# Performance work log

Hardware: AMD Instinct MI355X
Metric: run time of the kernel (lower is better)

Reference implementation:

```python
import jax, jax.numpy as jnp
import numpy as np

B, N, D = 8, 500, 256
H, W = 480, 640
NUM_CORNERS = 500
MATCH_RADIUS = 1.0
SCORE_RADIUS = 8
BETA = (1.0, 1.0, 1.0)


def _rodrigues(aa):
    theta = jnp.linalg.norm(aa, axis=-1, keepdims=True)
    k = aa / jnp.maximum(theta, 1e-8)
    kx, ky, kz = k[..., 0], k[..., 1], k[..., 2]
    z = jnp.zeros_like(kx)
    Km = jnp.stack([jnp.stack([z, -kz, ky], -1),
                    jnp.stack([kz, z, -kx], -1),
                    jnp.stack([-ky, kx, z], -1)], -2)
    th = theta[..., None]
    return jnp.eye(3) + jnp.sin(th) * Km + (1. - jnp.cos(th)) * (Km @ Km)


def setup_inputs() -> dict:
    key = jax.random.key(0)
    ks = jax.random.split(key, 8)
    descriptors = jax.random.normal(ks[0], (B, N, D), jnp.float32)
    points = jax.random.uniform(ks[1], (B, N, 2), jnp.float32, -1.0, 1.0)
    pointness = jax.random.uniform(ks[2], (B, 1, H, W), jnp.float32) * 0.98 + 0.01
    depths_dense = jax.random.uniform(ks[3], (B, 1, H, W), jnp.float32) * 4.0 + 1.0
    imgs = jax.random.uniform(ks[4], (B, 3, H, W), jnp.float32)
    aa = jax.random.normal(ks[5], (B, 3), jnp.float32) * 0.02
    t = jax.random.normal(ks[6], (B, 3), jnp.float32) * 0.05
    R = _rodrigues(aa)
    poses = jnp.tile(jnp.eye(4, dtype=jnp.float32), (B, 1, 1))
    poses = poses.at[:, :3, :3].set(R).at[:, :3, 3].set(t)
    Kmat = jnp.tile(jnp.array([[300., 0., W / 2.], [0., 300., H / 2.], [0., 0., 1.]], jnp.float32), (B, 1, 1))
    return {"descriptors": descriptors, "points": points, "pointness": pointness,
            "depths_dense": depths_dense, "poses": poses, "K": Kmat, "imgs": imgs}


def denormalize(pts, h, w):
    return jnp.stack([(pts[..., 0] + 1.) * 0.5 * (w - 1), (pts[..., 1] + 1.) * 0.5 * (h - 1)], -1)


def normalize_pix(pts, h, w):
    return jnp.stack([2. * pts[..., 0] / (w - 1) - 1., 2. * pts[..., 1] / (h - 1) - 1.], -1)


def bilinear_sample(img, px):  # img (H,W), px (...,2) pixel coords
    x = jnp.clip(px[..., 0], 0., W - 1.)
    y = jnp.clip(px[..., 1], 0., H - 1.)
    x0 = jnp.floor(x); y0 = jnp.floor(y)
    x1 = jnp.minimum(x0 + 1., W - 1.); y1 = jnp.minimum(y0 + 1., H - 1.)
    wx = x - x0; wy = y - y0
    x0i = x0.astype(jnp.int32); x1i = x1.astype(jnp.int32)
    y0i = y0.astype(jnp.int32); y1i = y1.astype(jnp.int32)
    v00 = img[y0i, x0i]; v01 = img[y0i, x1i]
    v10 = img[y1i, x0i]; v11 = img[y1i, x1i]
    return v00 * (1 - wx) * (1 - wy) + v01 * wx * (1 - wy) + v10 * (1 - wx) * wy + v11 * wx * wy


def pairwise_project(pts, depths, poses, Kmat):
    # pts (B,N,2) normalized; proj[i,j] = points of frame i projected into frame j
    px = denormalize(pts, H, W)
    d = jax.vmap(bilinear_sample)(depths[:, 0], px)  # (B,Np)
    Kinv = jnp.linalg.inv(Kmat)
    homog = jnp.concatenate([px, jnp.ones_like(px[..., :1])], -1)
    Xc = d[..., None] * jnp.einsum('bij,bnj->bni', Kinv, homog)
    Rm = poses[:, :3, :3]; t = poses[:, :3, 3]
    Xw = jnp.einsum('bij,bnj->bni', Rm, Xc) + t[:, None, :]
    diff = Xw[:, None, :, :] - t[None, :, None, :]           # (src,dst,Np,3)
    Xj = jnp.einsum('jba,ijnb->ijna', Rm, diff)              # R_j^T (Xw - t_j)
    uvw = jnp.einsum('jab,ijnb->ijna', Kmat, Xj)
    z = uvw[..., 2]
    zs = jnp.where(jnp.abs(z) < 1e-6, 1e-6, z)
    pn = normalize_pix(jnp.stack([uvw[..., 0] / zs, uvw[..., 1] / zs], -1), H, W)
    invis = (z <= 1e-6) | (jnp.abs(pn[..., 0]) > 1.) | (jnp.abs(pn[..., 1]) > 1.) | (d[:, None, :] <= 0.)
    return pn, invis


def conv2d_same(x, k):
    return jax.lax.conv_general_dilated(x, k[None, None].astype(x.dtype), (1, 1), 'SAME')


_SOBEL_X = np.array([[-1, 0, 1], [-2, 0, 2], [-1, 0, 1]], np.float32) / 8.


def _gauss_kernel(size=7, sigma=1.0):
    r = np.arange(size) - size // 2
    g = np.exp(-r ** 2 / (2 * sigma ** 2)); g /= g.sum()
    return np.outer(g, g).astype(np.float32)


_GAUSS = _gauss_kernel()


def gftt_response(gray):  # min-eigenvalue (Shi-Tomasi) corner response
    gx = conv2d_same(gray, jnp.asarray(_SOBEL_X))
    gy = conv2d_same(gray, jnp.asarray(_SOBEL_X.T))
    g = jnp.asarray(_GAUSS)
    dx2 = conv2d_same(gx * gx, g)
    dy2 = conv2d_same(gy * gy, g)
    dxy = conv2d_same(gx * gy, g)
    tr = dx2 + dy2
    det = dx2 * dy2 - dxy * dxy
    return 0.5 * (tr - jnp.sqrt(jnp.clip(tr * tr - 4. * det, 0.)))


def nms2d(x, k=5):
    mp = jax.lax.reduce_window(x, -jnp.inf, jax.lax.max, (1, 1, k, k), (1, 1, 1, 1), 'SAME')
    return x * (x == mp).astype(x.dtype)


def get_corners(imgs, depths, poses, Kmat):
    gray = (0.299 * imgs[:, 0] + 0.587 * imgs[:, 1] + 0.114 * imgs[:, 2])[:, None]
    c = nms2d(gftt_response(gray))
    r = SCORE_RADIUS
    blocks = c.reshape(B, 1, H // r, r, W // r, r)  # unfold/fold with stride==kernel
    bm = blocks.max(axis=(3, 5), keepdims=True)
    blocks = blocks * ((blocks > 0) & (blocks == bm)).astype(c.dtype)
    c = blocks.reshape(B, 1, H, W)
    vals, idx = jax.lax.top_k(c.reshape(B, -1), NUM_CORNERS)
    xs = (idx % W).astype(jnp.float32)
    ys = (idx // W).astype(jnp.float32)
    coords = normalize_pix(jnp.stack([xs, ys], -1), H, W)
    proj, invis = pairwise_project(coords, depths, poses, Kmat)
    proj = jnp.where(invis[..., None], -2.0, proj)
    combined = jnp.transpose(proj, (1, 0, 2, 3)).reshape(B, B * NUM_CORNERS, 2)  # per dst frame
    pix = jnp.round(denormalize(combined, H, W)).astype(jnp.int32)
    wq, hq = pix[..., 0], pix[..., 1]
    valid = wq >= 0
    v = jnp.tile(vals.reshape(-1), B).reshape(B, B * NUM_CORNERS)
    v = jnp.where(valid, v, 0.)
    hc = jnp.clip(hq, 0, H - 1)
    wc = jnp.clip(wq, 0, W - 1)
    bidx = jnp.broadcast_to(jnp.arange(B)[:, None], (B, B * NUM_CORNERS))
    target = jnp.zeros((B, H, W), imgs.dtype).at[bidx, hc, wc].max(v)
    target = nms2d(target[:, None])
    return (target > 0).astype(imgs.dtype)


def distinction_loss(desc):
    dn = desc / jnp.clip(jnp.linalg.norm(desc, axis=-1, keepdims=True), 1e-8)
    c = jnp.einsum('bnd,bmd->bnm', dn, dn)
    return jax.nn.relu(c).mean()


def match_loss(desc, points, proj, invis):
    p_src = denormalize(jax.lax.stop_gradient(points), H, W)  # (B,N,2)
    p_dst = denormalize(jax.lax.stop_gradient(proj), H, W)    # (src a, dst b, N, 2)
    diff = p_src[None, :, :, None, :] - p_dst[:, :, None, :, :]  # (a,b,n,m,2)
    m = (diff ** 2).sum(-1) <= MATCH_RADIUS ** 2
    m = m & (~invis)[:, :, :, None]                 # zero invisible rows
    n_idx = jnp.arange(N)
    m = m & (n_idx[:, None] < n_idx[None, :])       # triu(diagonal=1)
    dn = desc / jnp.clip(jnp.linalg.norm(desc, axis=-1, keepdims=True), 1e-8)
    cos = jnp.einsum('bnd,amd->abnm', dn, dn)       # cosine(desc[b,n], desc[a,m])
    mf = m.astype(desc.dtype)
    cnt = jnp.maximum(mf.sum(), 1.)
    return ((1. - cos) * mf).sum() / cnt


def bce(p, t):
    logp = jnp.maximum(jnp.log(p), -100.)
    log1p = jnp.maximum(jnp.log(1. - p), -100.)
    return -(t * logp + (1. - t) * log1p).mean()


def reference(descriptors, points, pointness, depths_dense, poses, K, imgs):
    distinction = distinction_loss(descriptors)
    target = get_corners(imgs, depths_dense, poses, K)
    cornerness = bce(pointness, target)
    proj, invis = pairwise_project(points, depths_dense, poses, K)
    match = match_loss(descriptors, points, proj, invis)
    return BETA[0] * distinction + BETA[1] * cornerness + BETA[2] * match
```

## Files before the change

kernel.cpp:

```cpp
#include <hip/hip_runtime.h>
#include <math.h>

#define BB 8
#define NN 500
#define DDIM 256
#define HH 480
#define WW 640
#define HWSZ (HH*WW)
#define BHW (BB*HWSZ)
#define NBLK 4800
#define NOVF 3392
#define NLIST (BB*NN*BB)
#define NBCE2 512
#define NCORR 125
#define NDM 66

#define PD_DIST  0
#define PD_MS    512
#define PD_MC    1024
#define PD_BCE   1536
#define PD_CORR  2560
#define PD_TOTAL 2688

typedef __attribute__((ext_vector_type(8))) short short8;
typedef __attribute__((ext_vector_type(4))) float f32x4;


static __device__ __forceinline__ float wredmaxf(float v) {
  #pragma unroll
  for (int o = 1; o < 64; o <<= 1) v = fmaxf(v, __shfl_xor(v, o, 64));
  return v;
}

static __device__ __forceinline__ double blockRedSum256(double v) {
  __shared__ double sp[4];
  __syncthreads();
  #pragma unroll
  for (int o = 32; o > 0; o >>= 1) v += __shfl_down(v, o, 64);
  int lane = threadIdx.x & 63, wid = threadIdx.x >> 6;
  if (lane == 0) sp[wid] = v;
  __syncthreads();
  double r = 0.0;
  if (threadIdx.x == 0) r = sp[0] + sp[1] + sp[2] + sp[3];
  return r;
}

static __device__ __forceinline__ unsigned short f2bf(float f) {
  unsigned u = __float_as_uint(f);
  return (unsigned short)((u + 0x7FFFu + ((u >> 16) & 1u)) >> 16);
}

static __device__ __forceinline__ float bilin(const float* __restrict__ img, float px, float py) {
  float x = fminf(fmaxf(px, 0.0f), 639.0f);
  float y = fminf(fmaxf(py, 0.0f), 479.0f);
  float x0 = floorf(x), y0 = floorf(y);
  float x1 = fminf(x0 + 1.0f, 639.0f);
  float y1 = fminf(y0 + 1.0f, 479.0f);
  float wx = x - x0, wy = y - y0;
  int x0i = (int)x0, x1i = (int)x1, y0i = (int)y0, y1i = (int)y1;
  float v00 = img[y0i*WW + x0i], v01 = img[y0i*WW + x1i];
  float v10 = img[y1i*WW + x0i], v11 = img[y1i*WW + x1i];
  return v00*(1.0f-wx)*(1.0f-wy) + v01*wx*(1.0f-wy) + v10*(1.0f-wx)*wy + v11*wx*wy;
}

static __device__ void src_compute(float px, float py, const float* __restrict__ dep,
                                   const float* __restrict__ poses, const float* __restrict__ Km,
                                   int bimg, float* Xw, float* dout) {
  float d = bilin(dep, px, py);
  const float* Kb = Km + bimg*9;
  double a00=Kb[0],a01=Kb[1],a02=Kb[2],a10=Kb[3],a11=Kb[4],a12=Kb[5],a20=Kb[6],a21=Kb[7],a22=Kb[8];
  double det = a00*(a11*a22-a12*a21) - a01*(a10*a22-a12*a20) + a02*(a10*a21-a11*a20);
  double id = 1.0/det;
  float i00=(float)((a11*a22-a12*a21)*id), i01=(float)((a02*a21-a01*a22)*id), i02=(float)((a01*a12-a02*a11)*id);
  float i10=(float)((a12*a20-a10*a22)*id), i11=(float)((a00*a22-a02*a20)*id), i12=(float)((a02*a10-a00*a12)*id);
  float i20=(float)((a10*a21-a11*a20)*id), i21=(float)((a01*a20-a00*a21)*id), i22=(float)((a00*a11-a01*a10)*id);
  float c0 = i00*px + i01*py + i02;
  float c1 = i10*px + i11*py + i12;
  float c2 = i20*px + i21*py + i22;
  float X0 = d*c0, X1 = d*c1, X2 = d*c2;
  const float* P = poses + bimg*16;
  Xw[0] = (P[0]*X0 + P[1]*X1 + P[2]*X2)  + P[3];
  Xw[1] = (P[4]*X0 + P[5]*X1 + P[6]*X2)  + P[7];
  Xw[2] = (P[8]*X0 + P[9]*X1 + P[10]*X2) + P[11];
  *dout = d;
}

static __device__ void project_to(const float* __restrict__ poses, const float* __restrict__ Km,
                                  int j, const float* Xw, float dsrc,
                                  float* pnx, float* pny, bool* invis) {
  const float* P = poses + j*16;
  float d0 = Xw[0]-P[3], d1 = Xw[1]-P[7], d2 = Xw[2]-P[11];
  float Xj0 = P[0]*d0 + P[4]*d1 + P[8]*d2;
  float Xj1 = P[1]*d0 + P[5]*d1 + P[9]*d2;
  float Xj2 = P[2]*d0 + P[6]*d1 + P[10]*d2;
  const float* Kb = Km + j*9;
  float u = Kb[0]*Xj0 + Kb[1]*Xj1 + Kb[2]*Xj2;
  float v = Kb[3]*Xj0 + Kb[4]*Xj1 + Kb[5]*Xj2;
  float z = Kb[6]*Xj0 + Kb[7]*Xj1 + Kb[8]*Xj2;
  float zs = (fabsf(z) < 1e-6f) ? 1e-6f : z;
  float pu = u/zs, pv = v/zs;
  float nx = 2.0f*pu/639.0f - 1.0f;
  float ny = 2.0f*pv/479.0f - 1.0f;
  *pnx = nx; *pny = ny;
  *invis = (z <= 1e-6f) || (fabsf(nx) > 1.0f) || (fabsf(ny) > 1.0f) || (dsrc <= 0.0f);
}


__global__ __launch_bounds__(256) void k_front(const float* __restrict__ imgs, float* __restrict__ resp,
                                               int* __restrict__ ovf, int* __restrict__ list,
                                               unsigned int* __restrict__ dnb_u, int* __restrict__ done,
                                               const float* __restrict__ desc, float* __restrict__ dn,
                                               unsigned short* __restrict__ dnb,
                                               const float* __restrict__ points, const float* __restrict__ depths,
                                               const float* __restrict__ poses, const float* __restrict__ Km,
                                               float* __restrict__ psrc, float* __restrict__ pdst,
                                               int* __restrict__ minv,
                                               const float* __restrict__ pn, double* __restrict__ pd) {
  __shared__ float smem[6536];
  __shared__ float Gw[7];
  int bid = blockIdx.x, tid = threadIdx.x;
  if (bid < 2400) {
    float* sgxy = smem;
    float* gray = smem + 2888;
    float* hxx  = smem + 2888;
    float* hyy  = hxx + 1216;
    float* hxy  = hyy + 1216;
    int b = bid / 300, r = bid % 300;
    int byi = r / 20, bxi = r % 20;
    int bx = bxi*32, by = byi*32;
    int tx = tid & 31, ty = tid >> 5;
    if (bid < 20) {
      int g = bid*256 + tid;
      if (g == 0) *done = 0;
      for (int e = g; e < BB*64; e += 20*256) ovf[e] = 0;
      for (int e = g; e < NLIST; e += 20*256) list[e] = -1;
      for (int e = g; e < 12288; e += 20*256) {
        int bi = e / 1536, rr2 = e % 1536;
        dnb_u[(bi*512 + 500)*128 + rr2] = 0u;
      }
    }
    if (tid < 7) {
      double g[7]; double s = 0.0;
      for (int q = 0; q < 7; q++) { double rr2 = (double)(q-3); g[q] = exp(-(rr2*rr2)/2.0); s += g[q]; }
      Gw[tid] = (float)(g[tid]/s);
    }
    const float* ib = imgs + (size_t)b*3*HWSZ;
    for (int ly = ty; ly < 40; ly += 8) {
      int Y = by - 4 + ly;
      bool yin = (Y >= 0 && Y < HH);
      for (int lx = tx; lx < 40; lx += 32) {
        int X = bx - 4 + lx;
        float v = 0.f;
        if (yin && X >= 0 && X < WW) {
          int p = Y*WW + X;
          v = 0.299f*ib[p] + 0.587f*ib[HWSZ+p] + 0.114f*ib[2*HWSZ+p];
        }
        gray[ly*41+lx] = v;
      }
    }
    __syncthreads();
    const float kxw[3][3] = {{-0.125f,0.f,0.125f},{-0.25f,0.f,0.25f},{-0.125f,0.f,0.125f}};
    for (int ly = ty; ly < 38; ly += 8) {
      int Y = by - 3 + ly;
      bool yin = (Y >= 0 && Y < HH);
      for (int lx = tx; lx < 38; lx += 32) {
        int X = bx - 3 + lx;
        float sx = 0.f, sy = 0.f;
        #pragma unroll
        for (int i = 0; i < 3; i++)
          #pragma unroll
          for (int j = 0; j < 3; j++) {
            float v = gray[(ly+i)*41 + (lx+j)];
            sx += kxw[i][j]*v;
            sy += kxw[j][i]*v;
          }
        bool in = yin && (X >= 0 && X < WW);
        int e = ly*38 + lx;
        sgxy[e*2]   = in ? sx : 0.f;
        sgxy[e*2+1] = in ? sy : 0.f;
      }
    }
    __syncthreads();
    for (int rr2 = ty; rr2 < 38; rr2 += 8) {
      int base = (rr2*38 + tx)*2;
      float axx = 0.f, ayy = 0.f, axy = 0.f;
      #pragma unroll
      for (int j = 0; j < 7; j++) {
        float a = sgxy[base + j*2];
        float c = sgxy[base + j*2 + 1];
        float Gj = Gw[j];
        axx += Gj*(a*a); ayy += Gj*(c*c); axy += Gj*(a*c);
      }
      int e = rr2*32 + tx;
      hxx[e] = axx; hyy[e] = ayy; hxy[e] = axy;
    }
    __syncthreads();
    int r0 = ty*4;
    float axx[4] = {0,0,0,0}, ayy[4] = {0,0,0,0}, axy[4] = {0,0,0,0};
    #pragma unroll
    for (int rr2 = 0; rr2 < 10; rr2++) {
      int rr3 = r0 + rr2;
      float vxx = hxx[rr3*32+tx], vyy = hyy[rr3*32+tx], vxy = hxy[rr3*32+tx];
      #pragma unroll
      for (int o = 0; o < 4; o++) {
        int i = rr2 - o;
        if (i >= 0 && i <= 6) {
          float Gi = Gw[i];
          axx[o] += Gi*vxx; ayy[o] += Gi*vyy; axy[o] += Gi*vxy;
        }
      }
    }
    #pragma unroll
    for (int o = 0; o < 4; o++) {
      float tr = axx[o] + ayy[o];
      float det = axx[o]*ayy[o] - axy[o]*axy[o];
      float disc = fmaxf(tr*tr - 4.0f*det, 0.f);
      int y = by + r0 + o;
      resp[(size_t)b*HWSZ + y*WW + (bx+tx)] = 0.5f*(tr - sqrtf(disc));
    }
  } else if (bid < 3400) {
    int row = (bid - 2400)*4 + (tid >> 6);
    int lane = tid & 63;
    float4 v4 = *(const float4*)&desc[(size_t)row*DDIM + lane*4];
    float s = v4.x*v4.x + v4.y*v4.y + v4.z*v4.z + v4.w*v4.w;
    #pragma unroll
    for (int o = 32; o > 0; o >>= 1) s += __shfl_down(s, o, 64);
    s = __shfl(s, 0, 64);
    float den = fmaxf(sqrtf(s), 1e-8f);
    float4 o4 = make_float4(v4.x/den, v4.y/den, v4.z/den, v4.w/den);
    *(float4*)&dn[(size_t)row*DDIM + lane*4] = o4;
    int pr = (row/500)*512 + (row%500);
    unsigned lo = (unsigned)f2bf(o4.x) | ((unsigned)f2bf(o4.y) << 16);
    unsigned hi = (unsigned)f2bf(o4.z) | ((unsigned)f2bf(o4.w) << 16);
    *(uint2*)&dnb[(size_t)pr*DDIM + lane*4] = make_uint2(lo, hi);
  } else if (bid < 3416) {
    int t = (bid - 3400)*256 + tid;
    if (t < BB*NN) {
      int a = t / NN, m = t % NN;
      float p0 = points[t*2], p1 = points[t*2+1];
      float px = (p0 + 1.0f)*0.5f*639.0f;
      float py = (p1 + 1.0f)*0.5f*479.0f;
      float Xw[3], d;
      src_compute(px, py, depths + (size_t)a*HWSZ, poses, Km, a, Xw, &d);
      psrc[t*2] = px; psrc[t*2+1] = py;
      for (int b = 0; b < BB; b++) {
        float nx, ny; bool inv;
        project_to(poses, Km, b, Xw, d, &nx, &ny, &inv);
        int o = (a*BB + b)*NN + m;
        pdst[o*2]   = (nx + 1.0f)*0.5f*639.0f;
        pdst[o*2+1] = (ny + 1.0f)*0.5f*479.0f;
        minv[o] = inv ? 1 : 0;
      }
    }
  } else {
    int blk = bid - 3416;
    int g = blk*256 + tid;
    double l = 0.0;
    for (int q = g; q < BHW/4; q += NBCE2*256) {
      float4 v = ((const float4*)pn)[q];
      l -= (double)fmaxf(logf(1.f - v.x), -100.f);
      l -= (double)fmaxf(logf(1.f - v.y), -100.f);
      l -= (double)fmaxf(logf(1.f - v.z), -100.f);
      l -= (double)fmaxf(logf(1.f - v.w), -100.f);
    }
    double s = blockRedSum256(l);
    if (tid == 0) pd[PD_BCE + blk] = s;
  }
}

__global__ __launch_bounds__(256) void k_mid(const float* __restrict__ resp, float* __restrict__ cv,
                                             int* __restrict__ ci, float* __restrict__ cvo,
                                             int* __restrict__ cio, int* __restrict__ ovf,
                                             float* __restrict__ target,
                                             const float* __restrict__ psrc, const float* __restrict__ pdst,
                                             const int* __restrict__ minv, const float* __restrict__ dn,
                                             const short* __restrict__ dnb, double* __restrict__ pd) {
  __shared__ float sbuf[3508];
  int bid = blockIdx.x, tid = threadIdx.x;
  if (bid < NDM) {
    int w = tid >> 6, lane = tid & 63;
    int gw = bid*4 + w;
    int r16 = lane & 15, koff = (lane >> 4)*8;
    double dsum = 0.0;
    for (int j = 0; j < 16; j++) {
      int jb = gw*16 + j;
      int b = jb / 528, t = jb % 528;
      int I = (int)((sqrtf(8.f*(float)t + 1.f) - 1.f)*0.5f);
      while ((I+1)*(I+2)/2 <= t) I++;
      while (I*(I+1)/2 > t) I--;
      int J = t - I*(I+1)/2;
      const short* bp = dnb + (size_t)b*512*DDIM;
      const short* ap = bp + (I*16 + r16)*DDIM + koff;
      const short* cp = bp + (J*16 + r16)*DDIM + koff;
      f32x4 acc = {0.f, 0.f, 0.f, 0.f};
      #pragma unroll
      for (int kk = 0; kk < 8; kk++) {
        short8 af = *(const short8*)(ap + kk*32);
        short8 bf = *(const short8*)(cp + kk*32);
        acc = __builtin_amdgcn_mfma_f32_16x16x32_bf16(af, bf, acc, 0, 0, 0);
      }
      float ls = fmaxf(acc[0],0.f) + fmaxf(acc[1],0.f) + fmaxf(acc[2],0.f) + fmaxf(acc[3],0.f);
      dsum += (double)ls * ((I == J) ? 1.0 : 2.0);
    }
    double s = blockRedSum256(dsum);
    if (tid == 0) pd[PD_DIST + bid] = s;
  } else if (bid < NDM + 512) {
    int mbid = bid - NDM;
    float* spd = sbuf;
    float* ssrc = sbuf + 1000;
    int* sinv = (int*)(sbuf + 2000);
    int ab = mbid & 63; int b = ab % BB; int a = ab / BB;
    int ys = mbid >> 6;
    for (int e = tid; e < NN; e += 256) {
      spd[e*2]   = pdst[(ab*NN+e)*2];
      spd[e*2+1] = pdst[(ab*NN+e)*2+1];
      sinv[e]    = minv[ab*NN+e];
      ssrc[e*2]   = psrc[(b*NN+e)*2];
      ssrc[e*2+1] = psrc[(b*NN+e)*2+1];
    }
    __syncthreads();
    double lsum = 0.0, lcnt = 0.0;
    for (int mm = ys; mm < NN; mm += 8) {
      float px = spd[mm*2], py = spd[mm*2+1];
      for (int nn = tid; nn < mm; nn += 256) {
        if (sinv[nn]) continue;
        float dx = ssrc[nn*2]   - px;
        float dy = ssrc[nn*2+1] - py;
        if (dx*dx + dy*dy <= 1.0f) {
          const float* da = dn + ((size_t)a*NN + mm)*DDIM;
          const float* db = dn + ((size_t)b*NN + nn)*DDIM;
          float dot = 0.f;
          for (int q = 0; q < DDIM; q++) dot += db[q]*da[q];
          lsum += (double)(1.0f - dot);
          lcnt += 1.0;
        }
      }
    }
    double s = blockRedSum256(lsum);
    if (tid == 0) pd[PD_MS + mbid] = s;
    double c2 = blockRedSum256(lcnt);
    if (tid == 0) pd[PD_MC + mbid] = c2;
  } else {
    int nb = bid - (NDM + 512);
    int b = nb / 300, r = nb % 300;
    int byi = r / 20, bxi = r % 20;
    int bx = bxi*32, by = byi*32;
    float* s = sbuf;
    float* hm = sbuf + 1332;
    float* c32 = sbuf + 2484;
    const float* rp = resp + (size_t)b*HWSZ;
    for (int e = tid; e < 36*36; e += 256) {
      int ly = e/36, lx = e%36;
      int X = bx - 2 + lx, Y = by - 2 + ly;
      s[ly*37+lx] = (X>=0 && X<WW && Y>=0 && Y<HH) ? rp[Y*WW+X] : -INFINITY;
    }
    __syncthreads();
    for (int e = tid; e < 36*32; e += 256) {
      int rr = e >> 5, co = e & 31;
      int base = rr*37 + co;
      float m = s[base];
      m = fmaxf(m, s[base+1]); m = fmaxf(m, s[base+2]);
      m = fmaxf(m, s[base+3]); m = fmaxf(m, s[base+4]);
      hm[e] = m;
    }
    __syncthreads();
    for (int e = tid; e < 1024; e += 256) {
      int y = e >> 5, x = e & 31;
      float mp = hm[y*32+x];
      mp = fmaxf(mp, hm[(y+1)*32+x]); mp = fmaxf(mp, hm[(y+2)*32+x]);
      mp = fmaxf(mp, hm[(y+3)*32+x]); mp = fmaxf(mp, hm[(y+4)*32+x]);
      float v = s[(y+2)*37 + (x+2)];
      c32[e] = (v == mp) ? v : 0.f;
      target[(size_t)b*HWSZ + (by+y)*WW + (bx+x)] = 0.f;
    }
    __syncthreads();
    int wv = tid >> 6, lane = tid & 63;
    int ly8 = lane >> 3, lx8 = lane & 7;
    for (int q = 0; q < 4; q++) {
      int bb = wv*4 + q;
      int oy = (bb >> 2)*8, ox = (bb & 3)*8;
      float cval = c32[(oy+ly8)*32 + ox+lx8];
      float bm = wredmaxf(cval);
      bool win = (cval > 0.f) && (cval == bm);
      unsigned long long mask = __ballot(win);
      int BY = byi*4 + (bb >> 2), BX = bxi*4 + (bb & 3);
      int rblk = BY*80 + BX;
      int gidx = (by+oy+ly8)*WW + (bx+ox+lx8);
      if (mask == 0ull) {
        if (lane == 0) { cv[b*NBLK+rblk] = 0.f; ci[b*NBLK+rblk] = 0; }
      } else if (win) {
        int rank = __popcll(mask & ((1ull << lane) - 1ull));
        if (rank == 0) { cv[b*NBLK+rblk] = cval; ci[b*NBLK+rblk] = gidx; }
        else {
          int pos = atomicAdd(&ovf[b*64], 1);
          if (pos < NOVF) { cvo[b*NOVF+pos] = cval; cio[b*NOVF+pos] = gidx; }
        }
      }
    }
  }
}

__global__ __launch_bounds__(1024) void k_topscat(const float* __restrict__ cv, const int* __restrict__ ci,
                                                  const float* __restrict__ cvo, const int* __restrict__ cio,
                                                  const int* __restrict__ ovf,
                                                  const float* __restrict__ depths, const float* __restrict__ poses,
                                                  const float* __restrict__ Km,
                                                  unsigned int* __restrict__ target, int* __restrict__ list) {
  __shared__ unsigned int hist[16*257];
  __shared__ unsigned int histsum[256];
  __shared__ unsigned long long prefix_s;
  __shared__ int kk_s, fin_s, cgt_s, ceq_s;
  __shared__ float s_topv[NN];
  __shared__ int s_topi[NN];
  int b = blockIdx.x;
  int tid = threadIdx.x;
  int w257 = (tid >> 6)*257;
  int nval = min(ovf[b*64], NOVF);
  unsigned long long kreg[8];
  #pragma unroll
  for (int q = 0; q < 8; q++) {
    int e = tid + q*1024;
    float v = 0.f; unsigned int idx = 0u;
    if (e < NBLK) { v = cv[b*NBLK+e]; idx = (unsigned int)ci[b*NBLK+e]; }
    else if (e - NBLK < nval) { v = cvo[b*NOVF+e-NBLK]; idx = (unsigned int)cio[b*NOVF+e-NBLK]; }
    kreg[q] = ((unsigned long long)__float_as_uint(v) << 32) | (0xFFFFFFFFu - idx);
  }
  if (tid == 0) { prefix_s = 0ull; kk_s = NN; fin_s = -1; cgt_s = 0; ceq_s = 0; }
  for (int e = tid; e < 16*257; e += 1024) hist[e] = 0u;
  __syncthreads();
  for (int round = 0; round < 8; round++) {
    int shift = 56 - 8*round;
    unsigned long long prefix = prefix_s;
    int kk = kk_s;
    unsigned long long himask = (round == 0) ? 0ull : (~0ull << (shift + 8));
    #pragma unroll
    for (int q = 0; q < 8; q++)
      if ((kreg[q] & himask) == prefix)
        atomicAdd(&hist[w257 + (unsigned int)((kreg[q] >> shift) & 255ull)], 1u);
    __syncthreads();
    if (tid < 256) {
      unsigned s = 0u;
      #pragma unroll
      for (int ww = 0; ww < 16; ww++) s += hist[ww*257 + tid];
      histsum[tid] = s;
    }
    __syncthreads();
    for (int e = tid; e < 16*257; e += 1024) hist[e] = 0u;
    if (tid < 64) {
      int l = tid;
      unsigned s0 = histsum[l], s1 = histsum[64+l], s2 = histsum[128+l], s3 = histsum[192+l];
      #pragma unroll
      for (int off = 1; off < 64; off <<= 1) {
        unsigned t0 = __shfl_down(s0, off, 64), t1 = __shfl_down(s1, off, 64);
        unsigned t2 = __shfl_down(s2, off, 64), t3 = __shfl_down(s3, off, 64);
        if (l + off < 64) { s0 += t0; s1 += t1; s2 += t2; s3 += t3; }
      }
      unsigned S1 = __shfl(s1, 0, 64), S2 = __shfl(s2, 0, 64), S3 = __shfl(s3, 0, 64);
      unsigned suf0 = s0 + S1 + S2 + S3, suf1 = s1 + S2 + S3, suf2 = s2 + S3, suf3 = s3;
      int best = -1;
      if      (suf3 >= (unsigned)kk) best = 192 + l;
      else if (suf2 >= (unsigned)kk) best = 128 + l;
      else if (suf1 >= (unsigned)kk) best = 64 + l;
      else if (suf0 >= (unsigned)kk) best = l;
      #pragma unroll
      for (int off = 1; off < 64; off <<= 1) best = max(best, __shfl_xor(best, off, 64));
      if (l == (best & 63)) {
        int seg = best >> 6;
        unsigned sufb = (seg == 3) ? suf3 : ((seg == 2) ? suf2 : ((seg == 1) ? suf1 : suf0));
        unsigned c = histsum[best];
        int Sn = (int)(sufb - c);
        int kkn = kk - Sn;
        prefix_s = prefix | ((unsigned long long)best << shift);
        kk_s = kkn;
        if (kkn == (int)c) fin_s = shift;
      }
    }
    __syncthreads();
    if (fin_s >= 0) break;
  }
  int sg = (fin_s > 0) ? fin_s : 0;
  unsigned long long prefix = prefix_s;
  int kk = kk_s;
  unsigned long long low = (sg > 0) ? ((1ull << sg) - 1ull) : 0ull;
  unsigned long long Tfull = prefix | low;
  unsigned long long mhi = ~low;
  int lane = tid & 63;
  unsigned long long lmask = (1ull << lane) - 1ull;
  #pragma unroll
  for (int q = 0; q < 8; q++) {
    unsigned long long key = kreg[q];
    bool gt = key > Tfull;
    bool eq = !gt && ((key & mhi) == prefix);
    unsigned long long mg = __ballot(gt);
    unsigned long long me = __ballot(eq);
    int slot = -1;
    if (mg != 0ull) {
      int ldr = __ffsll((long long)mg) - 1;
      int baseg = 0;
      if (lane == ldr) baseg = atomicAdd(&cgt_s, (int)__popcll(mg));
      baseg = __shfl(baseg, ldr, 64);
      if (gt) slot = baseg + (int)__popcll(mg & lmask);
    }
    if (me != 0ull) {
      int ldr = __ffsll((long long)me) - 1;
      int basee = 0;
      if (lane == ldr) basee = atomicAdd(&ceq_s, (int)__popcll(me));
      basee = __shfl(basee, ldr, 64);
      if (eq) {
        int p = basee + (int)__popcll(me & lmask);
        if (p < kk) slot = (NN-1) - p;
      }
    }
    if (slot >= 0) {
      s_topv[slot] = __uint_as_float((unsigned int)(key >> 32));
      s_topi[slot] = (int)(0xFFFFFFFFu - (unsigned int)(key & 0xFFFFFFFFull));
    }
  }
  __syncthreads();
  if (tid < NN) {
    float val = s_topv[tid];
    if (val > 0.f) {
      int idx = s_topi[tid];
      float xs = (float)(idx % WW), ys = (float)(idx / WW);
      float cx = 2.0f*xs/639.0f - 1.0f;
      float cy = 2.0f*ys/479.0f - 1.0f;
      float px = (cx + 1.0f)*0.5f*639.0f;
      float py = (cy + 1.0f)*0.5f*479.0f;
      float Xw[3], d;
      src_compute(px, py, depths + (size_t)b*HWSZ, poses, Km, b, Xw, &d);
      int tglob = b*NN + tid;
      for (int j = 0; j < BB; j++) {
        float nx, ny; bool inv;
        project_to(poses, Km, j, Xw, d, &nx, &ny, &inv);
        if (inv) { nx = -2.0f; ny = -2.0f; }
        float fx = rintf((nx + 1.0f)*0.5f*639.0f);
        float fy = rintf((ny + 1.0f)*0.5f*479.0f);
        int wq = (int)fx, hq = (int)fy;
        if (wq < 0) continue;
        int hc = min(max(hq, 0), HH-1), wc = min(max(wq, 0), WW-1);
        int p = j*HWSZ + hc*WW + wc;
        unsigned int old = atomicMax(&target[p], __float_as_uint(val));
        if (old == 0u) list[tglob*BB + j] = p;
      }
    }
  }
}

__global__ __launch_bounds__(256) void k_last(const int* __restrict__ list, const float* __restrict__ target,
                                              const float* __restrict__ pn, double* __restrict__ pd,
                                              int* __restrict__ done, float* __restrict__ out) {
  __shared__ int lastf;
  int blk = blockIdx.x, tid = threadIdx.x;
  int g = blk*256 + tid;
  double l = 0.0;
  if (g < NLIST) {
    int p = list[g];
    if (p >= 0) {
      int j = p / HWSZ, pix = p % HWSZ;
      int y = pix / WW, x = pix % WW;
      const float* tb = target + (size_t)j*HWSZ;
      float v = tb[pix];
      float mp = -INFINITY;
      for (int dy = -2; dy <= 2; dy++) {
        int yy = y + dy; if (yy < 0 || yy >= HH) continue;
        for (int dx = -2; dx <= 2; dx++) {
          int xx = x + dx; if (xx < 0 || xx >= WW) continue;
          mp = fmaxf(mp, tb[yy*WW+xx]);
        }
      }
      if (v > 0.f && v == mp) {
        float pv = pn[p];
        l = (double)(-fmaxf(logf(pv), -100.f)) + (double)fmaxf(logf(1.f - pv), -100.f);
      }
    }
  }
  double s = blockRedSum256(l);
  if (tid == 0) {
    pd[PD_CORR + blk] = s;
    __threadfence();
    int t = atomicAdd(done, 1);
    lastf = (t == NCORR - 1) ? 1 : 0;
  }
  __syncthreads();
  if (lastf) {
    __threadfence();
    double l2;
    l2 = 0.0; for (int i = tid; i < NDM;   i += 256) l2 += pd[PD_DIST + i];
    double dist = blockRedSum256(l2);
    l2 = 0.0; for (int i = tid; i < 512;   i += 256) l2 += pd[PD_MS + i];
    double ms = blockRedSum256(l2);
    l2 = 0.0; for (int i = tid; i < 512;   i += 256) l2 += pd[PD_MC + i];
    double mc = blockRedSum256(l2);
    l2 = 0.0; for (int i = tid; i < NBCE2; i += 256) l2 += pd[PD_BCE + i];
    double bce = blockRedSum256(l2);
    l2 = 0.0; for (int i = tid; i < NCORR; i += 256) l2 += pd[PD_CORR + i];
    double corr = blockRedSum256(l2);
    if (tid == 0) {
      float distf = (float)(dist / (double)(BB*NN*NN));
      float cornf = (float)((bce + corr) / (double)BHW);
      float cntf  = fmaxf((float)mc, 1.0f);
      float matchf = (float)ms / cntf;
      out[0] = distf + cornf + matchf;
    }
  }
}


extern "C" void kernel_launch(void* const* d_in, const int* in_sizes, int n_in,
                              void* d_out, int out_size, void* d_ws, size_t ws_size,
                              hipStream_t stream) {
  (void)in_sizes; (void)n_in; (void)out_size; (void)ws_size;
  const float* desc      = (const float*)d_in[0];
  const float* points    = (const float*)d_in[1];
  const float* pointness = (const float*)d_in[2];
  const float* depths    = (const float*)d_in[3];
  const float* poses     = (const float*)d_in[4];
  const float* Kmat      = (const float*)d_in[5];
  const float* imgs      = (const float*)d_in[6];
  float* out = (float*)d_out;

  double* pd = (double*)d_ws;
  float* f = (float*)(pd + PD_TOTAL);
  float* bufA = f;
  float* bufC = bufA + (size_t)BHW;
  float* cv_main = bufC + (size_t)BHW;
  int*   ci_main = (int*)(cv_main + BB*NBLK);
  float* cv_ovf  = (float*)(ci_main + BB*NBLK);
  int*   ci_ovf  = (int*)(cv_ovf + BB*NOVF);
  int*   ovf     = (int*)(ci_ovf + BB*NOVF);
  float* psrc = (float*)(ovf + BB*64);
  float* pdst = psrc + BB*NN*2;
  int*   minv = (int*)(pdst + BB*BB*NN*2);
  float* dn   = (float*)(minv + BB*BB*NN);
  int*   list = (int*)(dn + (size_t)BB*NN*DDIM);
  unsigned short* dnb = (unsigned short*)(list + NLIST);
  int*   done = (int*)(dnb + (size_t)BB*512*DDIM);

  k_front  <<<3928, 256, 0, stream>>>(imgs, bufA, ovf, list, (unsigned int*)dnb, done,
                                      desc, dn, dnb, points, depths, poses, Kmat,
                                      psrc, pdst, minv, pointness, pd);
  k_mid    <<<NDM + 512 + 2400, 256, 0, stream>>>(bufA, cv_main, ci_main, cv_ovf, ci_ovf, ovf, bufC,
                                                  psrc, pdst, minv, dn, (const short*)dnb, pd);
  k_topscat<<<BB, 1024, 0, stream>>>(cv_main, ci_main, cv_ovf, ci_ovf, ovf,
                                     depths, poses, Kmat, (unsigned int*)bufC, list);
  k_last   <<<NCORR, 256, 0, stream>>>(list, bufC, pointness, pd, done, out);
}
```

Before: 109.6 us.

## Fuse corner NMS into response kernel and move match/distinction blocks to final kernel

The response tile computation now uses a halo of 2 pixels and recomputes the response over a 36x36 region, so the 5x5 non-max suppression and per-8x8 block candidate selection happen in the same kernel, removing the full-size response buffer write and read and one kernel launch. The distinction MFMA blocks and match-loss blocks move from the removed middle kernel into the final kernel, which now counts all of its blocks for the last-block reduction. The cost is extra recomputation of the halo response and more shared memory per block, and the match/distinction work now runs after the serial top-k kernel instead of alongside it.

```diff
diff --git a/kernel.cpp b/kernel.cpp
--- a/kernel.cpp
+++ b/kernel.cpp
@@ -14,6 +14,7 @@
 #define NBCE2 512
 #define NCORR 125
 #define NDM 66
+#define NLAST (NDM + 512 + NCORR)
 
 #define PD_DIST  0
 #define PD_MS    512
@@ -106,7 +107,9 @@
 }
 
 
-__global__ __launch_bounds__(256) void k_front(const float* __restrict__ imgs, float* __restrict__ resp,
+__global__ __launch_bounds__(256) void k_front(const float* __restrict__ imgs,
+                                               float* __restrict__ cv, int* __restrict__ ci,
+                                               float* __restrict__ cvo, int* __restrict__ cio,
                                                int* __restrict__ ovf, int* __restrict__ list,
                                                unsigned int* __restrict__ dnb_u, int* __restrict__ done,
                                                const float* __restrict__ desc, float* __restrict__ dn,
@@ -115,20 +118,23 @@
                                                const float* __restrict__ poses, const float* __restrict__ Km,
                                                float* __restrict__ psrc, float* __restrict__ pdst,
                                                int* __restrict__ minv,
-                                               const float* __restrict__ pn, double* __restrict__ pd) {
-  __shared__ float smem[6536];
+                                               const float* __restrict__ pn, double* __restrict__ pd,
+                                               float* __restrict__ target) {
+  __shared__ float smem[8064];
   __shared__ float Gw[7];
   int bid = blockIdx.x, tid = threadIdx.x;
   if (bid < 2400) {
     float* sgxy = smem;
-    float* gray = smem + 2888;
-    float* hxx  = smem + 2888;
-    float* hyy  = hxx + 1216;
-    float* hxy  = hyy + 1216;
+    float* gray = smem + 3528;
+    float* hxx  = smem + 3528;
+    float* hyy  = hxx + 1512;
+    float* hxy  = hyy + 1512;
+    float* s    = smem;
+    float* hm   = smem + 1332;
+    float* c32  = smem + 2484;
     int b = bid / 300, r = bid % 300;
     int byi = r / 20, bxi = r % 20;
     int bx = bxi*32, by = byi*32;
-    int tx = tid & 31, ty = tid >> 5;
     if (bid < 20) {
       int g = bid*256 + tid;
       if (g == 0) *done = 0;
@@ -140,93 +146,125 @@
       }
     }
     if (tid < 7) {
-      double g[7]; double s = 0.0;
-      for (int q = 0; q < 7; q++) { double rr2 = (double)(q-3); g[q] = exp(-(rr2*rr2)/2.0); s += g[q]; }
-      Gw[tid] = (float)(g[tid]/s);
+      double g[7]; double sm = 0.0;
+      for (int q = 0; q < 7; q++) { double rr2 = (double)(q-3); g[q] = exp(-(rr2*rr2)/2.0); sm += g[q]; }
+      Gw[tid] = (float)(g[tid]/sm);
     }
     const float* ib = imgs + (size_t)b*3*HWSZ;
-    for (int ly = ty; ly < 40; ly += 8) {
-      int Y = by - 4 + ly;
-      bool yin = (Y >= 0 && Y < HH);
-      for (int lx = tx; lx < 40; lx += 32) {
-        int X = bx - 4 + lx;
-        float v = 0.f;
-        if (yin && X >= 0 && X < WW) {
-          int p = Y*WW + X;
-          v = 0.299f*ib[p] + 0.587f*ib[HWSZ+p] + 0.114f*ib[2*HWSZ+p];
+    for (int e = tid; e < 44*44; e += 256) {
+      int ly = e/44, lx = e%44;
+      int X = bx - 6 + lx, Y = by - 6 + ly;
+      float v = 0.f;
+      if (X>=0 && X<WW && Y>=0 && Y<HH) {
+        int p = Y*WW + X;
+        v = 0.299f*ib[p] + 0.587f*ib[HWSZ+p] + 0.114f*ib[2*HWSZ+p];
+      }
+      gray[ly*45+lx] = v;
+    }
+    __syncthreads();
+    const float kxw[3][3] = {{-0.125f,0.f,0.125f},{-0.25f,0.f,0.25f},{-0.125f,0.f,0.125f}};
+    for (int e = tid; e < 42*42; e += 256) {
+      int ly = e/42, lx = e%42;
+      int X = bx - 5 + lx, Y = by - 5 + ly;
+      float sx = 0.f, sy = 0.f;
+      #pragma unroll
+      for (int i = 0; i < 3; i++)
+        #pragma unroll
+        for (int j = 0; j < 3; j++) {
+          float v = gray[(ly+i)*45 + (lx+j)];
+          sx += kxw[i][j]*v;
+          sy += kxw[j][i]*v;
         }
-        gray[ly*41+lx] = v;
-      }
-    }
-    __syncthreads();
-    const float kxw[3][3] = {{-0.125f,0.f,0.125f},{-0.25f,0.f,0.25f},{-0.125f,0.f,0.125f}};
-    for (int ly = ty; ly < 38; ly += 8) {
-      int Y = by - 3 + ly;
-      bool yin = (Y >= 0 && Y < HH);
-      for (int lx = tx; lx < 38; lx += 32) {
-        int X = bx - 3 + lx;
-        float sx = 0.f, sy = 0.f;
-        #pragma unroll
-        for (int i = 0; i < 3; i++)
-          #pragma unroll
-          for (int j = 0; j < 3; j++) {
-            float v = gray[(ly+i)*41 + (lx+j)];
-            sx += kxw[i][j]*v;
-            sy += kxw[j][i]*v;
-          }
-        bool in = yin && (X >= 0 && X < WW);
-        int e = ly*38 + lx;
-        sgxy[e*2]   = in ? sx : 0.f;
-        sgxy[e*2+1] = in ? sy : 0.f;
-      }
-    }
-    __syncthreads();
-    for (int rr2 = ty; rr2 < 38; rr2 += 8) {
-      int base = (rr2*38 + tx)*2;
+      bool in = (X>=0 && X<WW && Y>=0 && Y<HH);
+      sgxy[e*2]   = in ? sx : 0.f;
+      sgxy[e*2+1] = in ? sy : 0.f;
+    }
+    __syncthreads();
+    for (int e = tid; e < 42*36; e += 256) {
+      int rr2 = e/36, c = e%36;
+      int base = (rr2*42 + c)*2;
       float axx = 0.f, ayy = 0.f, axy = 0.f;
       #pragma unroll
       for (int j = 0; j < 7; j++) {
         float a = sgxy[base + j*2];
-        float c = sgxy[base + j*2 + 1];
+        float cc = sgxy[base + j*2 + 1];
         float Gj = Gw[j];
-        axx += Gj*(a*a); ayy += Gj*(c*c); axy += Gj*(a*c);
-      }
-      int e = rr2*32 + tx;
+        axx += Gj*(a*a); ayy += Gj*(cc*cc); axy += Gj*(a*cc);
+      }
       hxx[e] = axx; hyy[e] = ayy; hxy[e] = axy;
     }
     __syncthreads();
-    int r0 = ty*4;
-    float axx[4] = {0,0,0,0}, ayy[4] = {0,0,0,0}, axy[4] = {0,0,0,0};
-    #pragma unroll
-    for (int rr2 = 0; rr2 < 10; rr2++) {
-      int rr3 = r0 + rr2;
-      float vxx = hxx[rr3*32+tx], vyy = hyy[rr3*32+tx], vxy = hxy[rr3*32+tx];
-      #pragma unroll
-      for (int o = 0; o < 4; o++) {
-        int i = rr2 - o;
-        if (i >= 0 && i <= 6) {
+    for (int e = tid; e < 36*36; e += 256) {
+      int rr2 = e/36, c = e%36;
+      int X = bx - 2 + c, Y = by - 2 + rr2;
+      float val = -INFINITY;
+      if (X>=0 && X<WW && Y>=0 && Y<HH) {
+        float axx = 0.f, ayy = 0.f, axy = 0.f;
+        #pragma unroll
+        for (int i = 0; i < 7; i++) {
           float Gi = Gw[i];
-          axx[o] += Gi*vxx; ayy[o] += Gi*vyy; axy[o] += Gi*vxy;
+          int hb = (rr2+i)*36 + c;
+          axx += Gi*hxx[hb]; ayy += Gi*hyy[hb]; axy += Gi*hxy[hb];
         }
-      }
-    }
-    #pragma unroll
-    for (int o = 0; o < 4; o++) {
-      float tr = axx[o] + ayy[o];
-      float det = axx[o]*ayy[o] - axy[o]*axy[o];
-      float disc = fmaxf(tr*tr - 4.0f*det, 0.f);
-      int y = by + r0 + o;
-      resp[(size_t)b*HWSZ + y*WW + (bx+tx)] = 0.5f*(tr - sqrtf(disc));
+        float tr = axx + ayy;
+        float det = axx*ayy - axy*axy;
+        float disc = fmaxf(tr*tr - 4.0f*det, 0.f);
+        val = 0.5f*(tr - sqrtf(disc));
+      }
+      s[rr2*37 + c] = val;
+    }
+    __syncthreads();
+    for (int e = tid; e < 36*32; e += 256) {
+      int rr2 = e >> 5, co = e & 31;
+      int base = rr2*37 + co;
+      float m = s[base];
+      m = fmaxf(m, s[base+1]); m = fmaxf(m, s[base+2]);
+      m = fmaxf(m, s[base+3]); m = fmaxf(m, s[base+4]);
+      hm[e] = m;
+    }
+    __syncthreads();
+    for (int e = tid; e < 1024; e += 256) {
+      int y = e >> 5, x = e & 31;
+      float mp = hm[y*32+x];
+      mp = fmaxf(mp, hm[(y+1)*32+x]); mp = fmaxf(mp, hm[(y+2)*32+x]);
+      mp = fmaxf(mp, hm[(y+3)*32+x]); mp = fmaxf(mp, hm[(y+4)*32+x]);
+      float v = s[(y+2)*37 + (x+2)];
+      c32[e] = (v == mp) ? v : 0.f;
+      target[(size_t)b*HWSZ + (by+y)*WW + (bx+x)] = 0.f;
+    }
+    __syncthreads();
+    int wv = tid >> 6, lane = tid & 63;
+    int ly8 = lane >> 3, lx8 = lane & 7;
+    for (int q = 0; q < 4; q++) {
+      int bb = wv*4 + q;
+      int oy = (bb >> 2)*8, ox = (bb & 3)*8;
+      float cval = c32[(oy+ly8)*32 + ox+lx8];
+      float bm = wredmaxf(cval);
+      bool win = (cval > 0.f) && (cval == bm);
+      unsigned long long mask = __ballot(win);
+      int BY = byi*4 + (bb >> 2), BX = bxi*4 + (bb & 3);
+      int rblk = BY*80 + BX;
+      int gidx = (by+oy+ly8)*WW + (bx+ox+lx8);
+      if (mask == 0ull) {
+        if (lane == 0) { cv[b*NBLK+rblk] = 0.f; ci[b*NBLK+rblk] = 0; }
+      } else if (win) {
+        int rank = __popcll(mask & ((1ull << lane) - 1ull));
+        if (rank == 0) { cv[b*NBLK+rblk] = cval; ci[b*NBLK+rblk] = gidx; }
+        else {
+          int pos = atomicAdd(&ovf[b*64], 1);
+          if (pos < NOVF) { cvo[b*NOVF+pos] = cval; cio[b*NOVF+pos] = gidx; }
+        }
+      }
     }
   } else if (bid < 3400) {
     int row = (bid - 2400)*4 + (tid >> 6);
     int lane = tid & 63;
     float4 v4 = *(const float4*)&desc[(size_t)row*DDIM + lane*4];
-    float s = v4.x*v4.x + v4.y*v4.y + v4.z*v4.z + v4.w*v4.w;
+    float sacc = v4.x*v4.x + v4.y*v4.y + v4.z*v4.z + v4.w*v4.w;
     #pragma unroll
-    for (int o = 32; o > 0; o >>= 1) s += __shfl_down(s, o, 64);
-    s = __shfl(s, 0, 64);
-    float den = fmaxf(sqrtf(s), 1e-8f);
+    for (int o = 32; o > 0; o >>= 1) sacc += __shfl_down(sacc, o, 64);
+    sacc = __shfl(sacc, 0, 64);
+    float den = fmaxf(sqrtf(sacc), 1e-8f);
     float4 o4 = make_float4(v4.x/den, v4.y/den, v4.z/den, v4.w/den);
     *(float4*)&dn[(size_t)row*DDIM + lane*4] = o4;
     int pr = (row/500)*512 + (row%500);
@@ -263,140 +301,8 @@
       l -= (double)fmaxf(logf(1.f - v.z), -100.f);
       l -= (double)fmaxf(logf(1.f - v.w), -100.f);
     }
-    double s = blockRedSum256(l);
-    if (tid == 0) pd[PD_BCE + blk] = s;
-  }
-}
-
-__global__ __launch_bounds__(256) void k_mid(const float* __restrict__ resp, float* __restrict__ cv,
-                                             int* __restrict__ ci, float* __restrict__ cvo,
-                                             int* __restrict__ cio, int* __restrict__ ovf,
-                                             float* __restrict__ target,
-                                             const float* __restrict__ psrc, const float* __restrict__ pdst,
-                                             const int* __restrict__ minv, const float* __restrict__ dn,
-                                             const short* __restrict__ dnb, double* __restrict__ pd) {
-  __shared__ float sbuf[3508];
-  int bid = blockIdx.x, tid = threadIdx.x;
-  if (bid < NDM) {
-    int w = tid >> 6, lane = tid & 63;
-    int gw = bid*4 + w;
-    int r16 = lane & 15, koff = (lane >> 4)*8;
-    double dsum = 0.0;
-    for (int j = 0; j < 16; j++) {
-      int jb = gw*16 + j;
-      int b = jb / 528, t = jb % 528;
-      int I = (int)((sqrtf(8.f*(float)t + 1.f) - 1.f)*0.5f);
-      while ((I+1)*(I+2)/2 <= t) I++;
-      while (I*(I+1)/2 > t) I--;
-      int J = t - I*(I+1)/2;
-      const short* bp = dnb + (size_t)b*512*DDIM;
-      const short* ap = bp + (I*16 + r16)*DDIM + koff;
-      const short* cp = bp + (J*16 + r16)*DDIM + koff;
-      f32x4 acc = {0.f, 0.f, 0.f, 0.f};
-      #pragma unroll
-      for (int kk = 0; kk < 8; kk++) {
-        short8 af = *(const short8*)(ap + kk*32);
-        short8 bf = *(const short8*)(cp + kk*32);
-        acc = __builtin_amdgcn_mfma_f32_16x16x32_bf16(af, bf, acc, 0, 0, 0);
-      }
-      float ls = fmaxf(acc[0],0.f) + fmaxf(acc[1],0.f) + fmaxf(acc[2],0.f) + fmaxf(acc[3],0.f);
-      dsum += (double)ls * ((I == J) ? 1.0 : 2.0);
-    }
-    double s = blockRedSum256(dsum);
-    if (tid == 0) pd[PD_DIST + bid] = s;
-  } else if (bid < NDM + 512) {
-    int mbid = bid - NDM;
-    float* spd = sbuf;
-    float* ssrc = sbuf + 1000;
-    int* sinv = (int*)(sbuf + 2000);
-    int ab = mbid & 63; int b = ab % BB; int a = ab / BB;
-    int ys = mbid >> 6;
-    for (int e = tid; e < NN; e += 256) {
-      spd[e*2]   = pdst[(ab*NN+e)*2];
-      spd[e*2+1] = pdst[(ab*NN+e)*2+1];
-      sinv[e]    = minv[ab*NN+e];
-      ssrc[e*2]   = psrc[(b*NN+e)*2];
-      ssrc[e*2+1] = psrc[(b*NN+e)*2+1];
-    }
-    __syncthreads();
-    double lsum = 0.0, lcnt = 0.0;
-    for (int mm = ys; mm < NN; mm += 8) {
-      float px = spd[mm*2], py = spd[mm*2+1];
-      for (int nn = tid; nn < mm; nn += 256) {
-        if (sinv[nn]) continue;
-        float dx = ssrc[nn*2]   - px;
-        float dy = ssrc[nn*2+1] - py;
-        if (dx*dx + dy*dy <= 1.0f) {
-          const float* da = dn + ((size_t)a*NN + mm)*DDIM;
-          const float* db = dn + ((size_t)b*NN + nn)*DDIM;
-          float dot = 0.f;
-          for (int q = 0; q < DDIM; q++) dot += db[q]*da[q];
-          lsum += (double)(1.0f - dot);
-          lcnt += 1.0;
-        }
-      }
-    }
-    double s = blockRedSum256(lsum);
-    if (tid == 0) pd[PD_MS + mbid] = s;
-    double c2 = blockRedSum256(lcnt);
-    if (tid == 0) pd[PD_MC + mbid] = c2;
-  } else {
-    int nb = bid - (NDM + 512);
-    int b = nb / 300, r = nb % 300;
-    int byi = r / 20, bxi = r % 20;
-    int bx = bxi*32, by = byi*32;
-    float* s = sbuf;
-    float* hm = sbuf + 1332;
-    float* c32 = sbuf + 2484;
-    const float* rp = resp + (size_t)b*HWSZ;
-    for (int e = tid; e < 36*36; e += 256) {
-      int ly = e/36, lx = e%36;
-      int X = bx - 2 + lx, Y = by - 2 + ly;
-      s[ly*37+lx] = (X>=0 && X<WW && Y>=0 && Y<HH) ? rp[Y*WW+X] : -INFINITY;
-    }
-    __syncthreads();
-    for (int e = tid; e < 36*32; e += 256) {
-      int rr = e >> 5, co = e & 31;
-      int base = rr*37 + co;
-      float m = s[base];
-      m = fmaxf(m, s[base+1]); m = fmaxf(m, s[base+2]);
-      m = fmaxf(m, s[base+3]); m = fmaxf(m, s[base+4]);
-      hm[e] = m;
-    }
-    __syncthreads();
-    for (int e = tid; e < 1024; e += 256) {
-      int y = e >> 5, x = e & 31;
-      float mp = hm[y*32+x];
-      mp = fmaxf(mp, hm[(y+1)*32+x]); mp = fmaxf(mp, hm[(y+2)*32+x]);
-      mp = fmaxf(mp, hm[(y+3)*32+x]); mp = fmaxf(mp, hm[(y+4)*32+x]);
-      float v = s[(y+2)*37 + (x+2)];
-      c32[e] = (v == mp) ? v : 0.f;
-      target[(size_t)b*HWSZ + (by+y)*WW + (bx+x)] = 0.f;
-    }
-    __syncthreads();
-    int wv = tid >> 6, lane = tid & 63;
-    int ly8 = lane >> 3, lx8 = lane & 7;
-    for (int q = 0; q < 4; q++) {
-      int bb = wv*4 + q;
-      int oy = (bb >> 2)*8, ox = (bb & 3)*8;
-      float cval = c32[(oy+ly8)*32 + ox+lx8];
-      float bm = wredmaxf(cval);
-      bool win = (cval > 0.f) && (cval == bm);
-      unsigned long long mask = __ballot(win);
-      int BY = byi*4 + (bb >> 2), BX = bxi*4 + (bb & 3);
-      int rblk = BY*80 + BX;
-      int gidx = (by+oy+ly8)*WW + (bx+ox+lx8);
-      if (mask == 0ull) {
-        if (lane == 0) { cv[b*NBLK+rblk] = 0.f; ci[b*NBLK+rblk] = 0; }
-      } else if (win) {
-        int rank = __popcll(mask & ((1ull << lane) - 1ull));
-        if (rank == 0) { cv[b*NBLK+rblk] = cval; ci[b*NBLK+rblk] = gidx; }
-        else {
-          int pos = atomicAdd(&ovf[b*64], 1);
-          if (pos < NOVF) { cvo[b*NOVF+pos] = cval; cio[b*NOVF+pos] = gidx; }
-        }
-      }
-    }
+    double sred = blockRedSum256(l);
+    if (tid == 0) pd[PD_BCE + blk] = sred;
   }
 }
 
@@ -546,40 +452,110 @@
   }
 }
 
-__global__ __launch_bounds__(256) void k_last(const int* __restrict__ list, const float* __restrict__ target,
+__global__ __launch_bounds__(256) void k_last(const float* __restrict__ psrc, const float* __restrict__ pdst,
+                                              const int* __restrict__ minv, const float* __restrict__ dn,
+                                              const short* __restrict__ dnb,
+                                              const int* __restrict__ list, const float* __restrict__ target,
                                               const float* __restrict__ pn, double* __restrict__ pd,
                                               int* __restrict__ done, float* __restrict__ out) {
+  __shared__ float sbuf[2500];
   __shared__ int lastf;
-  int blk = blockIdx.x, tid = threadIdx.x;
-  int g = blk*256 + tid;
-  double l = 0.0;
-  if (g < NLIST) {
-    int p = list[g];
-    if (p >= 0) {
-      int j = p / HWSZ, pix = p % HWSZ;
-      int y = pix / WW, x = pix % WW;
-      const float* tb = target + (size_t)j*HWSZ;
-      float v = tb[pix];
-      float mp = -INFINITY;
-      for (int dy = -2; dy <= 2; dy++) {
-        int yy = y + dy; if (yy < 0 || yy >= HH) continue;
-        for (int dx = -2; dx <= 2; dx++) {
-          int xx = x + dx; if (xx < 0 || xx >= WW) continue;
-          mp = fmaxf(mp, tb[yy*WW+xx]);
+  int bid = blockIdx.x, tid = threadIdx.x;
+  if (bid < NDM) {
+    int w = tid >> 6, lane = tid & 63;
+    int gw = bid*4 + w;
+    int r16 = lane & 15, koff = (lane >> 4)*8;
+    double dsum = 0.0;
+    for (int j = 0; j < 16; j++) {
+      int jb = gw*16 + j;
+      int b = jb / 528, t = jb % 528;
+      int I = (int)((sqrtf(8.f*(float)t + 1.f) - 1.f)*0.5f);
+      while ((I+1)*(I+2)/2 <= t) I++;
+      while (I*(I+1)/2 > t) I--;
+      int J = t - I*(I+1)/2;
+      const short* bp = dnb + (size_t)b*512*DDIM;
+      const short* ap = bp + (I*16 + r16)*DDIM + koff;
+      const short* cp = bp + (J*16 + r16)*DDIM + koff;
+      f32x4 acc = {0.f, 0.f, 0.f, 0.f};
+      #pragma unroll
+      for (int kk = 0; kk < 8; kk++) {
+        short8 af = *(const short8*)(ap + kk*32);
+        short8 bf = *(const short8*)(cp + kk*32);
+        acc = __builtin_amdgcn_mfma_f32_16x16x32_bf16(af, bf, acc, 0, 0, 0);
+      }
+      float ls = fmaxf(acc[0],0.f) + fmaxf(acc[1],0.f) + fmaxf(acc[2],0.f) + fmaxf(acc[3],0.f);
+      dsum += (double)ls * ((I == J) ? 1.0 : 2.0);
+    }
+    double s = blockRedSum256(dsum);
+    if (tid == 0) pd[PD_DIST + bid] = s;
+  } else if (bid < NDM + 512) {
+    int mbid = bid - NDM;
+    float* spd = sbuf;
+    float* ssrc = sbuf + 1000;
+    int* sinv = (int*)(sbuf + 2000);
+    int ab = mbid & 63; int b = ab % BB; int a = ab / BB;
+    int ys = mbid >> 6;
+    for (int e = tid; e < NN; e += 256) {
+      spd[e*2]   = pdst[(ab*NN+e)*2];
+      spd[e*2+1] = pdst[(ab*NN+e)*2+1];
+      sinv[e]    = minv[ab*NN+e];
+      ssrc[e*2]   = psrc[(b*NN+e)*2];
+      ssrc[e*2+1] = psrc[(b*NN+e)*2+1];
+    }
+    __syncthreads();
+    double lsum = 0.0, lcnt = 0.0;
+    for (int mm = ys; mm < NN; mm += 8) {
+      float px = spd[mm*2], py = spd[mm*2+1];
+      for (int nn = tid; nn < mm; nn += 256) {
+        if (sinv[nn]) continue;
+        float dx = ssrc[nn*2]   - px;
+        float dy = ssrc[nn*2+1] - py;
+        if (dx*dx + dy*dy <= 1.0f) {
+          const float* da = dn + ((size_t)a*NN + mm)*DDIM;
+          const float* db = dn + ((size_t)b*NN + nn)*DDIM;
+          float dot = 0.f;
+          for (int q = 0; q < DDIM; q++) dot += db[q]*da[q];
+          lsum += (double)(1.0f - dot);
+          lcnt += 1.0;
         }
       }
-      if (v > 0.f && v == mp) {
-        float pv = pn[p];
-        l = (double)(-fmaxf(logf(pv), -100.f)) + (double)fmaxf(logf(1.f - pv), -100.f);
-      }
-    }
-  }
-  double s = blockRedSum256(l);
+    }
+    double s = blockRedSum256(lsum);
+    if (tid == 0) pd[PD_MS + mbid] = s;
+    double c2 = blockRedSum256(lcnt);
+    if (tid == 0) pd[PD_MC + mbid] = c2;
+  } else {
+    int blk = bid - (NDM + 512);
+    int g = blk*256 + tid;
+    double l = 0.0;
+    if (g < NLIST) {
+      int p = list[g];
+      if (p >= 0) {
+        int j = p / HWSZ, pix = p % HWSZ;
+        int y = pix / WW, x = pix % WW;
+        const float* tb = target + (size_t)j*HWSZ;
+        float v = tb[pix];
+        float mp = -INFINITY;
+        for (int dy = -2; dy <= 2; dy++) {
+          int yy = y + dy; if (yy < 0 || yy >= HH) continue;
+          for (int dx = -2; dx <= 2; dx++) {
+            int xx = x + dx; if (xx < 0 || xx >= WW) continue;
+            mp = fmaxf(mp, tb[yy*WW+xx]);
+          }
+        }
+        if (v > 0.f && v == mp) {
+          float pv = pn[p];
+          l = (double)(-fmaxf(logf(pv), -100.f)) + (double)fmaxf(logf(1.f - pv), -100.f);
+        }
+      }
+    }
+    double s = blockRedSum256(l);
+    if (tid == 0) pd[PD_CORR + blk] = s;
+  }
   if (tid == 0) {
-    pd[PD_CORR + blk] = s;
     __threadfence();
     int t = atomicAdd(done, 1);
-    lastf = (t == NCORR - 1) ? 1 : 0;
+    lastf = (t == NLAST - 1) ? 1 : 0;
   }
   __syncthreads();
   if (lastf) {
@@ -621,8 +597,7 @@
 
   double* pd = (double*)d_ws;
   float* f = (float*)(pd + PD_TOTAL);
-  float* bufA = f;
-  float* bufC = bufA + (size_t)BHW;
+  float* bufC = f;
   float* cv_main = bufC + (size_t)BHW;
   int*   ci_main = (int*)(cv_main + BB*NBLK);
   float* cv_ovf  = (float*)(ci_main + BB*NBLK);
@@ -636,12 +611,12 @@
   unsigned short* dnb = (unsigned short*)(list + NLIST);
   int*   done = (int*)(dnb + (size_t)BB*512*DDIM);
 
-  k_front  <<<3928, 256, 0, stream>>>(imgs, bufA, ovf, list, (unsigned int*)dnb, done,
-                                      desc, dn, dnb, points, depths, poses, Kmat,
-                                      psrc, pdst, minv, pointness, pd);
-  k_mid    <<<NDM + 512 + 2400, 256, 0, stream>>>(bufA, cv_main, ci_main, cv_ovf, ci_ovf, ovf, bufC,
-                                                  psrc, pdst, minv, dn, (const short*)dnb, pd);
+  k_front  <<<3928, 256, 0, stream>>>(imgs, cv_main, ci_main, cv_ovf, ci_ovf, ovf, list,
+                                      (unsigned int*)dnb, done, desc, dn, dnb,
+                                      points, depths, poses, Kmat,
+                                      psrc, pdst, minv, pointness, pd, bufC);
   k_topscat<<<BB, 1024, 0, stream>>>(cv_main, ci_main, cv_ovf, ci_ovf, ovf,
                                      depths, poses, Kmat, (unsigned int*)bufC, list);
-  k_last   <<<NCORR, 256, 0, stream>>>(list, bufC, pointness, pd, done, out);
-}
+  k_last   <<<NLAST, 256, 0, stream>>>(psrc, pdst, minv, dn, (const short*)dnb,
+                                       list, bufC, pointness, pd, done, out);
+}
```

After: 118.3 us. 1.08x slower.
